# Kernel optimization log

Measured on AMD Instinct MI355X. Metric: run time of the kernel, lower is better.

The kernel has to match this reference:

```python
import jax, jax.numpy as jnp
import numpy as np

B, S = 256, 512          # batch, seqlen
M = 128                  # memory_size
DK = 128                 # memory_key_state_dim == q_embed_dim == final_fc_dim
DV = 256                 # memory_value_state_dim == qa_embed_dim
NQ = 10000               # n_question
FC = 128                 # final_fc_dim


def _kaiming(key, shape):
    fan_in = shape[-1]
    return jax.random.normal(key, shape, dtype=jnp.float32) * np.float32(np.sqrt(2.0 / fan_in))


def setup_inputs() -> dict:
    key = jax.random.key(0)
    ks = jax.random.split(key, 12)
    q_data = jax.random.randint(ks[0], (B, S), 0, NQ + 1)
    qa_data = jax.random.randint(ks[1], (B, S), 0, 2 * NQ + 1)
    # embedding tables (padding_idx=0 -> zero row)
    q_embed_table = _kaiming(ks[2], (NQ + 1, DK)).at[0].set(0.0)
    qa_embed_table = _kaiming(ks[3], (2 * NQ + 1, DV)).at[0].set(0.0)
    memory_key = _kaiming(ks[4], (M, DK))
    init_memory_value = _kaiming(ks[5], (M, DV))
    W_erase = _kaiming(ks[6], (DV, DV)); b_erase = jnp.zeros((DV,), jnp.float32)
    W_add = _kaiming(ks[7], (DV, DV)); b_add = jnp.zeros((DV,), jnp.float32)
    W_read = _kaiming(ks[8], (FC, DV + FC)); b_read = jnp.zeros((FC,), jnp.float32)
    W_pred = _kaiming(ks[9], (1, FC)); b_pred = jnp.zeros((1,), jnp.float32)
    return {
        "q_data": q_data, "qa_data": qa_data,
        "q_embed_table": q_embed_table, "qa_embed_table": qa_embed_table,
        "memory_key": memory_key, "init_memory_value": init_memory_value,
        "W_erase": W_erase, "b_erase": b_erase,
        "W_add": W_add, "b_add": b_add,
        "W_read": W_read, "b_read": b_read,
        "W_pred": W_pred, "b_pred": b_pred,
    }


def reference(q_data, qa_data, q_embed_table, qa_embed_table, memory_key,
              init_memory_value, W_erase, b_erase, W_add, b_add,
              W_read, b_read, W_pred, b_pred):
    batch = q_data.shape[0]
    qe = q_embed_table[q_data]      # [B,S,DK]
    qae = qa_embed_table[qa_data]   # [B,S,DV]

    def step(mem, inp):
        q_t, qa_t = inp  # [B,DK], [B,DV]
        # key addressing: tiny matmul + softmax
        w = jax.nn.softmax(q_t @ memory_key.T, axis=1)            # [B,M]
        # weighted read from value memory
        read = jnp.einsum('bm,bmd->bd', w, mem)                   # [B,DV]
        # gated erase/add write
        e = jax.nn.sigmoid(qa_t @ W_erase.T + b_erase)            # [B,DV]
        a = jnp.tanh(qa_t @ W_add.T + b_add)                      # [B,DV]
        mem = mem * (1.0 - w[:, :, None] * e[:, None, :]) + w[:, :, None] * a[:, None, :]
        return mem, read

    mem0 = jnp.broadcast_to(init_memory_value, (batch,) + init_memory_value.shape)
    _, reads = jax.lax.scan(step, mem0, (qe.transpose(1, 0, 2), qae.transpose(1, 0, 2)))
    reads = reads.transpose(1, 0, 2)                              # [B,S,DV]

    predict_input = jnp.concatenate([reads, qe], axis=-1)         # [B,S,DV+FC]
    h = jnp.tanh(predict_input @ W_read.T + b_read)               # [B,S,FC]
    logits = h @ W_pred.T + b_pred                                # [B,S,1]
    return logits[..., 0]
```

## Files before the change

kernel.cpp:

```cpp
#include <hip/hip_runtime.h>
#include <hip/hip_bf16.h>


#define BB    256
#define SS    512
#define MM    128
#define DKk   128
#define DVv   256

typedef float  f32x2  __attribute__((ext_vector_type(2)));
typedef float  f32x4  __attribute__((ext_vector_type(4)));
typedef short  bf16x8 __attribute__((ext_vector_type(8)));

static __device__ __forceinline__ unsigned short f2bf(float f) {
    unsigned u = __float_as_uint(f);
    unsigned r = (u + 0x7FFFu + ((u >> 16) & 1u)) >> 16;
    return (unsigned short)r;
}
static __device__ __forceinline__ float bf2f(unsigned short u) {
    return __uint_as_float(((unsigned)u) << 16);
}
static __device__ __forceinline__ float fast_tanh(float x) {
    float ex = __expf(2.f * x);
    return 1.f - 2.f / (ex + 1.f);
}
static __device__ __forceinline__ float fast_sigmoid(float x) {
    return 1.f / (1.f + __expf(-x));
}

__global__ __launch_bounds__(256) void kcvt(const float* __restrict__ qa_tab,
                                            const float* __restrict__ q_tab,
                                            const float* __restrict__ W_er,
                                            const float* __restrict__ W_ad,
                                            const float* __restrict__ W_rd,
                                            const float* __restrict__ mk,
                                            unsigned short* __restrict__ qa16,
                                            unsigned short* __restrict__ q16,
                                            unsigned short* __restrict__ wea16,
                                            unsigned short* __restrict__ wrd16,
                                            unsigned short* __restrict__ mk16,
                                            int n_qa, int n_q) {
    for (int i = blockIdx.x * 256 + threadIdx.x; i < n_qa; i += gridDim.x * 256)
        qa16[i] = f2bf(qa_tab[i]);
    for (int i = blockIdx.x * 256 + threadIdx.x; i < n_q; i += gridDim.x * 256)
        q16[i] = f2bf(q_tab[i]);
    for (int i = blockIdx.x * 256 + threadIdx.x; i < 65536; i += gridDim.x * 256) {
        wea16[i] = f2bf(W_er[i]);
        wea16[65536 + i] = f2bf(W_ad[i]);
    }
    for (int i = blockIdx.x * 256 + threadIdx.x; i < 49152; i += gridDim.x * 256)
        wrd16[i] = f2bf(W_rd[i]);
    for (int i = blockIdx.x * 256 + threadIdx.x; i < 16384; i += gridDim.x * 256)
        mk16[i] = f2bf(mk[i]);
}

__global__ __launch_bounds__(256) void k1_mfma(const int* __restrict__ q_data,
                                               const unsigned short* __restrict__ q16,
                                               const unsigned short* __restrict__ mk16,
                                               float* __restrict__ w_buf,
                                               int tcs, int tcm, int coff) {
    __shared__ __align__(16) unsigned short A_lds[128 * 64];
    __shared__ int qidx[128];
    int t = threadIdx.x;
    int row0 = blockIdx.x * 128;
    if (t < 128) {
        int rl = row0 + t;
        qidx[t] = q_data[(rl >> tcs) * SS + coff + (rl & tcm)];
    }
    int l = t & 63;
    int wid = t >> 6;
    f32x4 acc[2][8];
    #pragma unroll
    for (int i = 0; i < 2; ++i)
        #pragma unroll
        for (int j = 0; j < 8; ++j)
            acc[i][j] = (f32x4){0.f, 0.f, 0.f, 0.f};

    for (int ks = 0; ks < 128; ks += 64) {
        __syncthreads();
        #pragma unroll
        for (int p = 0; p < 4; ++p) {
            int U = p * 256 + t;
            int r = U >> 3, kb = U & 7;
            int kb_log = kb ^ (r & 7);
            int4 v = *reinterpret_cast<const int4*>(q16 + (size_t)qidx[r] * DKk + ks + kb_log * 8);
            *reinterpret_cast<int4*>(&A_lds[U * 8]) = v;
        }
        __syncthreads();
        #pragma unroll
        for (int ksub = 0; ksub < 2; ++ksub) {
            bf16x8 af[2];
            #pragma unroll
            for (int mi = 0; mi < 2; ++mi) {
                int r = wid * 32 + mi * 16 + (l & 15);
                int kb_log = ksub * 4 + (l >> 4);
                int pu = r * 8 + (kb_log ^ (r & 7));
                af[mi] = *reinterpret_cast<const bf16x8*>(&A_lds[pu * 8]);
            }
            #pragma unroll
            for (int nj = 0; nj < 8; ++nj) {
                int col = nj * 16 + (l & 15);
                bf16x8 bf = *reinterpret_cast<const bf16x8*>(
                    mk16 + (size_t)col * DKk + ks + ksub * 32 + (l >> 4) * 8);
                #pragma unroll
                for (int mi = 0; mi < 2; ++mi)
                    acc[mi][nj] = __builtin_amdgcn_mfma_f32_16x16x32_bf16(af[mi], bf, acc[mi][nj], 0, 0, 0);
            }
        }
    }
    #pragma unroll
    for (int mi = 0; mi < 2; ++mi) {
        #pragma unroll
        for (int reg = 0; reg < 4; ++reg) {
            float mx = acc[mi][0][reg];
            #pragma unroll
            for (int nj = 1; nj < 8; ++nj) mx = fmaxf(mx, acc[mi][nj][reg]);
            #pragma unroll
            for (int off = 1; off < 16; off <<= 1) mx = fmaxf(mx, __shfl_xor(mx, off, 64));
            float p[8], s = 0.f;
            #pragma unroll
            for (int nj = 0; nj < 8; ++nj) { p[nj] = __expf(acc[mi][nj][reg] - mx); s += p[nj]; }
            #pragma unroll
            for (int off = 1; off < 16; off <<= 1) s += __shfl_xor(s, off, 64);
            float inv = 1.f / s;
            int row = row0 + wid * 32 + mi * 16 + (l >> 4) * 4 + reg;
            #pragma unroll
            for (int nj = 0; nj < 8; ++nj)
                w_buf[(size_t)row * MM + nj * 16 + (l & 15)] = p[nj] * inv;
        }
    }
}

__global__ __launch_bounds__(256) void k2_ea_mfma(const int* __restrict__ qa_data,
                                                  const unsigned short* __restrict__ qa16,
                                                  const unsigned short* __restrict__ wea16,
                                                  const float* __restrict__ b_er,
                                                  const float* __restrict__ b_ad,
                                                  unsigned short* __restrict__ ea16,
                                                  int tcs, int tcm, int coff) {
    __shared__ __align__(16) unsigned short A_lds[128 * 64];
    __shared__ int qidx[128];
    int t = threadIdx.x;
    int rb = blockIdx.x >> 2, cb = blockIdx.x & 3;
    int row0 = rb * 128;
    if (t < 128) {
        int rl = row0 + t;
        qidx[t] = qa_data[(rl >> tcs) * SS + coff + (rl & tcm)];
    }
    int l = t & 63;
    int wid = t >> 6, wr = wid >> 1, wc = wid & 1;
    f32x4 acc[4][4];
    #pragma unroll
    for (int i = 0; i < 4; ++i)
        #pragma unroll
        for (int j = 0; j < 4; ++j)
            acc[i][j] = (f32x4){0.f, 0.f, 0.f, 0.f};

    for (int ks = 0; ks < 256; ks += 64) {
        __syncthreads();
        #pragma unroll
        for (int p = 0; p < 4; ++p) {
            int U = p * 256 + t;
            int r = U >> 3, kb = U & 7;
            int kb_log = kb ^ (r & 7);
            int4 v = *reinterpret_cast<const int4*>(qa16 + (size_t)qidx[r] * 256 + ks + kb_log * 8);
            *reinterpret_cast<int4*>(&A_lds[U * 8]) = v;
        }
        __syncthreads();
        #pragma unroll
        for (int ksub = 0; ksub < 2; ++ksub) {
            bf16x8 af[4];
            #pragma unroll
            for (int mi = 0; mi < 4; ++mi) {
                int r = wr * 64 + mi * 16 + (l & 15);
                int kb_log = ksub * 4 + (l >> 4);
                int pu = r * 8 + (kb_log ^ (r & 7));
                af[mi] = *reinterpret_cast<const bf16x8*>(&A_lds[pu * 8]);
            }
            #pragma unroll
            for (int nj = 0; nj < 4; ++nj) {
                int col = cb * 128 + wc * 64 + nj * 16 + (l & 15);
                bf16x8 bf = *reinterpret_cast<const bf16x8*>(
                    wea16 + (size_t)col * 256 + ks + ksub * 32 + (l >> 4) * 8);
                #pragma unroll
                for (int mi = 0; mi < 4; ++mi)
                    acc[mi][nj] = __builtin_amdgcn_mfma_f32_16x16x32_bf16(af[mi], bf, acc[mi][nj], 0, 0, 0);
            }
        }
    }
    #pragma unroll
    for (int nj = 0; nj < 4; ++nj) {
        int col = cb * 128 + wc * 64 + nj * 16 + (l & 15);
        bool is_e = (cb < 2);
        float bias = is_e ? b_er[col] : b_ad[col - 256];
        #pragma unroll
        for (int mi = 0; mi < 4; ++mi) {
            #pragma unroll
            for (int reg = 0; reg < 4; ++reg) {
                int rl = row0 + wr * 64 + mi * 16 + (l >> 4) * 4 + reg;
                float x = acc[mi][nj][reg] + bias;
                float y = is_e ? fast_sigmoid(x) : fast_tanh(x);
                ea16[(size_t)rl * 512 + col] = f2bf(y);
            }
        }
    }
}

__global__ __launch_bounds__(1024, 8) void k3_seq(const float* __restrict__ w_buf,
                                                  const unsigned short* __restrict__ ea16,
                                                  const float* __restrict__ init_mem,
                                                  float* __restrict__ state,
                                                  unsigned short* __restrict__ reads16,
                                                  int TC, int first, int last) {
    __shared__ float rdlds[8][8][128];
    int b    = blockIdx.x >> 1;
    int half = blockIdx.x & 1;
    int tid = threadIdx.x;
    int wv = tid >> 6, lane = tid & 63;
    int mq = wv >> 1;
    int dh = wv & 1;
    int dl = dh * 64 + lane;
    int d  = half * 128 + dl;
    int m0 = mq * 16;
    f32x2 mem[8];
    if (first) {
        #pragma unroll
        for (int i = 0; i < 8; ++i) {
            mem[i].x = init_mem[(size_t)(m0 + 2 * i) * DVv + d];
            mem[i].y = init_mem[(size_t)(m0 + 2 * i + 1) * DVv + d];
        }
    } else {
        #pragma unroll
        for (int i = 0; i < 8; ++i)
            mem[i] = *reinterpret_cast<const f32x2*>(&state[((size_t)b * DVv + d) * MM + m0 + 2 * i]);
    }
    size_t rb = (size_t)b * TC;
    unsigned wrow = (unsigned)__builtin_amdgcn_readfirstlane((int)((unsigned)rb * MM + m0));
    const f32x2* wbase2 = reinterpret_cast<const f32x2*>(w_buf + wrow);
    int tcl = TC - 1;

    f32x2 wA[8], wB[8];
    #pragma unroll
    for (int j = 0; j < 8; ++j) wA[j] = wbase2[j];
    #pragma unroll
    for (int j = 0; j < 8; ++j) wB[j] = wbase2[64 + j];

    for (int t0 = 0; t0 < TC; t0 += 8) {
        float e8[8], a8[8];
        #pragma unroll
        for (int g = 0; g < 8; ++g) {
            const unsigned short* ep = ea16 + (rb + t0 + g) * 512;
            e8[g] = bf2f(ep[d]);
            a8[g] = bf2f(ep[256 + d]);
        }
        #define K3_STEP(G, WCUR)                                                              \
        {                                                                                     \
            f32x2 rd; rd.x = 0.f; rd.y = 0.f;                                                 \
            f32x2 ne2; ne2.x = -e8[G]; ne2.y = -e8[G];                                        \
            f32x2 a2;  a2.x = a8[G];  a2.y = a8[G];                                           \
            _Pragma("unroll")                                                                 \
            for (int i = 0; i < 8; ++i) {                                                     \
                f32x2 tt;                                                                     \
                asm("v_pk_fma_f32 %0, %1, %2, %0" : "+v"(rd)     : "s"(WCUR[i]), "v"(mem[i]));\
                asm("v_pk_fma_f32 %0, %1, %2, %3" : "=v"(tt)     : "v"(ne2), "v"(mem[i]), "v"(a2)); \
                asm("v_pk_fma_f32 %0, %1, %2, %0" : "+v"(mem[i]) : "s"(WCUR[i]), "v"(tt));    \
            }                                                                                 \
            rdlds[G][mq][dl] = rd.x + rd.y;                                                   \
            int tp = t0 + G + 2; tp = (tp < tcl) ? tp : tcl;                                  \
            _Pragma("unroll")                                                                 \
            for (int j = 0; j < 8; ++j) WCUR[j] = wbase2[tp * 64 + j];                        \
        }
        K3_STEP(0, wA) K3_STEP(1, wB) K3_STEP(2, wA) K3_STEP(3, wB)
        K3_STEP(4, wA) K3_STEP(5, wB) K3_STEP(6, wA) K3_STEP(7, wB)
        #undef K3_STEP
        __syncthreads();
        {
            int g = tid >> 7, dd = tid & 127;
            float s = rdlds[g][0][dd] + rdlds[g][1][dd] + rdlds[g][2][dd] + rdlds[g][3][dd]
                    + rdlds[g][4][dd] + rdlds[g][5][dd] + rdlds[g][6][dd] + rdlds[g][7][dd];
            reads16[(rb + t0 + g) * DVv + half * 128 + dd] = f2bf(s);
        }
        __syncthreads();
    }
    if (!last) {
        #pragma unroll
        for (int i = 0; i < 8; ++i)
            *reinterpret_cast<f32x2*>(&state[((size_t)b * DVv + d) * MM + m0 + 2 * i]) = mem[i];
    }
}

__global__ __launch_bounds__(256) void k4_mfma(const int* __restrict__ q_data,
                                               const unsigned short* __restrict__ q16,
                                               const unsigned short* __restrict__ reads16,
                                               const unsigned short* __restrict__ wrd16,
                                               const float* __restrict__ b_rd,
                                               const float* __restrict__ W_pr,
                                               const float* __restrict__ b_pr,
                                               float* __restrict__ out,
                                               int tcs, int tcm, int coff) {
    __shared__ __align__(16) unsigned short A_lds[128 * 64];
    __shared__ int qidx[128];
    __shared__ float plds[2][128];
    int t = threadIdx.x;
    int row0 = blockIdx.x * 128;
    if (t < 128) {
        int rl = row0 + t;
        qidx[t] = q_data[(rl >> tcs) * SS + coff + (rl & tcm)];
    }
    int l = t & 63;
    int wid = t >> 6, wr = wid >> 1, wc = wid & 1;
    f32x4 acc[4][4];
    #pragma unroll
    for (int i = 0; i < 4; ++i)
        #pragma unroll
        for (int j = 0; j < 4; ++j)
            acc[i][j] = (f32x4){0.f, 0.f, 0.f, 0.f};

    for (int ks = 0; ks < 384; ks += 64) {
        __syncthreads();
        #pragma unroll
        for (int p = 0; p < 4; ++p) {
            int U = p * 256 + t;
            int r = U >> 3, kb = U & 7;
            int kb_log = kb ^ (r & 7);
            int kg = ks + kb_log * 8;
            const unsigned short* src = (kg < 256)
                ? (reads16 + (size_t)(row0 + r) * DVv + kg)
                : (q16 + (size_t)qidx[r] * DKk + (kg - 256));
            int4 v = *reinterpret_cast<const int4*>(src);
            *reinterpret_cast<int4*>(&A_lds[U * 8]) = v;
        }
        __syncthreads();
        #pragma unroll
        for (int ksub = 0; ksub < 2; ++ksub) {
            bf16x8 af[4];
            #pragma unroll
            for (int mi = 0; mi < 4; ++mi) {
                int r = wr * 64 + mi * 16 + (l & 15);
                int kb_log = ksub * 4 + (l >> 4);
                int pu = r * 8 + (kb_log ^ (r & 7));
                af[mi] = *reinterpret_cast<const bf16x8*>(&A_lds[pu * 8]);
            }
            #pragma unroll
            for (int nj = 0; nj < 4; ++nj) {
                int col = wc * 64 + nj * 16 + (l & 15);
                bf16x8 bf = *reinterpret_cast<const bf16x8*>(
                    wrd16 + (size_t)col * 384 + ks + ksub * 32 + (l >> 4) * 8);
                #pragma unroll
                for (int mi = 0; mi < 4; ++mi)
                    acc[mi][nj] = __builtin_amdgcn_mfma_f32_16x16x32_bf16(af[mi], bf, acc[mi][nj], 0, 0, 0);
            }
        }
    }
    float part[16];
    #pragma unroll
    for (int k = 0; k < 16; ++k) part[k] = 0.f;
    #pragma unroll
    for (int nj = 0; nj < 4; ++nj) {
        int col = wc * 64 + nj * 16 + (l & 15);
        float bias = b_rd[col];
        float wpr = W_pr[col];
        #pragma unroll
        for (int mi = 0; mi < 4; ++mi) {
            #pragma unroll
            for (int reg = 0; reg < 4; ++reg) {
                float h = fast_tanh(acc[mi][nj][reg] + bias);
                part[mi * 4 + reg] = fmaf(h, wpr, part[mi * 4 + reg]);
            }
        }
    }
    #pragma unroll
    for (int k = 0; k < 16; ++k) {
        #pragma unroll
        for (int off = 1; off < 16; off <<= 1)
            part[k] += __shfl_xor(part[k], off, 64);
    }
    if ((l & 15) == 0) {
        #pragma unroll
        for (int mi = 0; mi < 4; ++mi)
            #pragma unroll
            for (int reg = 0; reg < 4; ++reg) {
                int row = wr * 64 + mi * 16 + (l >> 4) * 4 + reg;
                plds[wc][row] = part[mi * 4 + reg];
            }
    }
    __syncthreads();
    if (t < 128) {
        float s = plds[0][t] + plds[1][t] + b_pr[0];
        int rl = row0 + t;
        out[(rl >> tcs) * SS + coff + (rl & tcm)] = s;
    }
}

extern "C" void kernel_launch(void* const* d_in, const int* in_sizes, int n_in,
                              void* d_out, int out_size, void* d_ws, size_t ws_size,
                              hipStream_t stream) {
    const int*   q_data   = (const int*)d_in[0];
    const int*   qa_data  = (const int*)d_in[1];
    const float* q_tab    = (const float*)d_in[2];
    const float* qa_tab   = (const float*)d_in[3];
    const float* mk       = (const float*)d_in[4];
    const float* init_mem = (const float*)d_in[5];
    const float* W_er     = (const float*)d_in[6];
    const float* b_er     = (const float*)d_in[7];
    const float* W_ad     = (const float*)d_in[8];
    const float* b_ad     = (const float*)d_in[9];
    const float* W_rd     = (const float*)d_in[10];
    const float* b_rd     = (const float*)d_in[11];
    const float* W_pr     = (const float*)d_in[12];
    const float* b_pr     = (const float*)d_in[13];
    float* out = (float*)d_out;

    const size_t state_f = (size_t)BB * MM * DVv;
    const size_t qa16_n  = (size_t)in_sizes[3];
    const size_t q16_n   = (size_t)in_sizes[2];
    const size_t wea16_n = 131072;
    const size_t wrd16_n = 49152;
    const size_t mk16_n  = 16384;
    const size_t bf16_f  = (qa16_n + q16_n + wea16_n + wrd16_n + mk16_n) / 2 + 32;

    size_t avail_f = ws_size / 4;
    int TC = 8;
    {
        const int cand[] = {256, 128, 64, 32, 16, 8};
        for (int i = 0; i < 6; ++i) {
            size_t need = state_f + bf16_f + (size_t)BB * cand[i] * (MM + 256 + 128);
            if (need <= avail_f) { TC = cand[i]; break; }
        }
    }
    int NC = SS / TC;
    int tcs = __builtin_ctz(TC);
    int tcm = TC - 1;

    float* ws      = (float*)d_ws;
    float* state   = ws;
    float* w_buf   = state + state_f;
    unsigned short* ea16    = (unsigned short*)(w_buf + (size_t)BB * TC * MM);
    unsigned short* reads16 = ea16 + (size_t)BB * TC * 512;
    unsigned short* qa16  = reads16 + (size_t)BB * TC * DVv;
    unsigned short* q16   = qa16 + qa16_n;
    unsigned short* wea16 = q16 + q16_n;
    unsigned short* wrd16 = wea16 + wea16_n;
    unsigned short* mk16  = wrd16 + wrd16_n;

    kcvt<<<1024, 256, 0, stream>>>(qa_tab, q_tab, W_er, W_ad, W_rd, mk,
                                   qa16, q16, wea16, wrd16, mk16,
                                   (int)qa16_n, (int)q16_n);
    for (int c = 0; c < NC; ++c) {
        int coff = c * TC;
        int rows = BB * TC;
        k2_ea_mfma<<<(rows / 128) * 4, 256, 0, stream>>>(qa_data, qa16, wea16, b_er, b_ad,
                                                         ea16, tcs, tcm, coff);
        k1_mfma<<<rows / 128, 256, 0, stream>>>(q_data, q16, mk16, w_buf, tcs, tcm, coff);
        k3_seq<<<2 * BB, 1024, 0, stream>>>(w_buf, ea16, init_mem, state, reads16,
                                            TC, c == 0, c == NC - 1);
        k4_mfma<<<rows / 128, 256, 0, stream>>>(q_data, q16, reads16, wrd16, b_rd, W_pr, b_pr,
                                                out, tcs, tcm, coff);
    }
}
```

Measured before the change: 595.0 us.

## Reduce k3 read partials with wave shuffles instead of LDS and block barriers

Restructures the sequential memory-update kernel from 1024-thread blocks (two per batch row) to 256-thread blocks (eight per batch row). The lane layout changes so that all eight m-slices of a d column sit in one wave. Per-step read partial sums are now combined with xor shuffles inside the wave, which removes the LDS buffer and both __syncthreads per 8-step group. The cost is that attention weights become per-lane vector loads (VGPR operands) instead of uniform scalar loads, so register and memory traffic for w rises.

Measured after the change: 913.9 us. 53.6% more time.

```diff
diff --git a/kernel.cpp b/kernel.cpp
--- a/kernel.cpp
+++ b/kernel.cpp
@@ -206,21 +206,19 @@
     }
 }
 
-__global__ __launch_bounds__(1024, 8) void k3_seq(const float* __restrict__ w_buf,
-                                                  const unsigned short* __restrict__ ea16,
-                                                  const float* __restrict__ init_mem,
-                                                  float* __restrict__ state,
-                                                  unsigned short* __restrict__ reads16,
-                                                  int TC, int first, int last) {
-    __shared__ float rdlds[8][8][128];
-    int b    = blockIdx.x >> 1;
-    int half = blockIdx.x & 1;
+__global__ __launch_bounds__(256, 6) void k3_seq(const float* __restrict__ w_buf,
+                                                 const unsigned short* __restrict__ ea16,
+                                                 const float* __restrict__ init_mem,
+                                                 float* __restrict__ state,
+                                                 unsigned short* __restrict__ reads16,
+                                                 int TC, int first, int last) {
     int tid = threadIdx.x;
     int wv = tid >> 6, lane = tid & 63;
-    int mq = wv >> 1;
-    int dh = wv & 1;
-    int dl = dh * 64 + lane;
-    int d  = half * 128 + dl;
+    int b    = blockIdx.x >> 3;
+    int dblk = blockIdx.x & 7;
+    int mq   = lane >> 3;
+    int dsub = lane & 7;
+    int d  = dblk * 32 + wv * 8 + dsub;
     int m0 = mq * 16;
     f32x2 mem[8];
     if (first) {
@@ -235,15 +233,19 @@
             mem[i] = *reinterpret_cast<const f32x2*>(&state[((size_t)b * DVv + d) * MM + m0 + 2 * i]);
     }
     size_t rb = (size_t)b * TC;
-    unsigned wrow = (unsigned)__builtin_amdgcn_readfirstlane((int)((unsigned)rb * MM + m0));
-    const f32x2* wbase2 = reinterpret_cast<const f32x2*>(w_buf + wrow);
     int tcl = TC - 1;
 
     f32x2 wA[8], wB[8];
-    #pragma unroll
-    for (int j = 0; j < 8; ++j) wA[j] = wbase2[j];
-    #pragma unroll
-    for (int j = 0; j < 8; ++j) wB[j] = wbase2[64 + j];
+    #define WLOAD(WARR, T)                                                                  \
+    {                                                                                       \
+        const float* wsrc = w_buf + (rb + (size_t)(T)) * MM + m0;                           \
+        *reinterpret_cast<f32x4*>(&WARR[0]) = *reinterpret_cast<const f32x4*>(wsrc);        \
+        *reinterpret_cast<f32x4*>(&WARR[2]) = *reinterpret_cast<const f32x4*>(wsrc + 4);    \
+        *reinterpret_cast<f32x4*>(&WARR[4]) = *reinterpret_cast<const f32x4*>(wsrc + 8);    \
+        *reinterpret_cast<f32x4*>(&WARR[6]) = *reinterpret_cast<const f32x4*>(wsrc + 12);   \
+    }
+    WLOAD(wA, 0)
+    WLOAD(wB, 1)
 
     for (int t0 = 0; t0 < TC; t0 += 8) {
         float e8[8], a8[8];
@@ -253,6 +255,7 @@
             e8[g] = bf2f(ep[d]);
             a8[g] = bf2f(ep[256 + d]);
         }
+        float rds[8];
         #define K3_STEP(G, WCUR)                                                              \
         {                                                                                     \
             f32x2 rd; rd.x = 0.f; rd.y = 0.f;                                                 \
@@ -261,27 +264,32 @@
             _Pragma("unroll")                                                                 \
             for (int i = 0; i < 8; ++i) {                                                     \
                 f32x2 tt;                                                                     \
-                asm("v_pk_fma_f32 %0, %1, %2, %0" : "+v"(rd)     : "s"(WCUR[i]), "v"(mem[i]));\
+                asm("v_pk_fma_f32 %0, %1, %2, %0" : "+v"(rd)     : "v"(WCUR[i]), "v"(mem[i]));\
                 asm("v_pk_fma_f32 %0, %1, %2, %3" : "=v"(tt)     : "v"(ne2), "v"(mem[i]), "v"(a2)); \
-                asm("v_pk_fma_f32 %0, %1, %2, %0" : "+v"(mem[i]) : "s"(WCUR[i]), "v"(tt));    \
+                asm("v_pk_fma_f32 %0, %1, %2, %0" : "+v"(mem[i]) : "v"(WCUR[i]), "v"(tt));    \
             }                                                                                 \
-            rdlds[G][mq][dl] = rd.x + rd.y;                                                   \
+            rds[G] = rd.x + rd.y;                                                             \
             int tp = t0 + G + 2; tp = (tp < tcl) ? tp : tcl;                                  \
-            _Pragma("unroll")                                                                 \
-            for (int j = 0; j < 8; ++j) WCUR[j] = wbase2[tp * 64 + j];                        \
+            WLOAD(WCUR, tp)                                                                   \
         }
         K3_STEP(0, wA) K3_STEP(1, wB) K3_STEP(2, wA) K3_STEP(3, wB)
         K3_STEP(4, wA) K3_STEP(5, wB) K3_STEP(6, wA) K3_STEP(7, wB)
         #undef K3_STEP
-        __syncthreads();
-        {
-            int g = tid >> 7, dd = tid & 127;
-            float s = rdlds[g][0][dd] + rdlds[g][1][dd] + rdlds[g][2][dd] + rdlds[g][3][dd]
-                    + rdlds[g][4][dd] + rdlds[g][5][dd] + rdlds[g][6][dd] + rdlds[g][7][dd];
-            reads16[(rb + t0 + g) * DVv + half * 128 + dd] = f2bf(s);
-        }
-        __syncthreads();
-    }
+        #pragma unroll
+        for (int g = 0; g < 8; ++g) {
+            float v = rds[g];
+            v += __shfl_xor(v, 8, 64);
+            v += __shfl_xor(v, 16, 64);
+            v += __shfl_xor(v, 32, 64);
+            rds[g] = v;
+        }
+        if (mq == 0) {
+            #pragma unroll
+            for (int g = 0; g < 8; ++g)
+                reads16[(rb + t0 + g) * DVv + d] = f2bf(rds[g]);
+        }
+    }
+    #undef WLOAD
     if (!last) {
         #pragma unroll
         for (int i = 0; i < 8; ++i)
@@ -452,8 +460,8 @@
         k2_ea_mfma<<<(rows / 128) * 4, 256, 0, stream>>>(qa_data, qa16, wea16, b_er, b_ad,
                                                          ea16, tcs, tcm, coff);
         k1_mfma<<<rows / 128, 256, 0, stream>>>(q_data, q16, mk16, w_buf, tcs, tcm, coff);
-        k3_seq<<<2 * BB, 1024, 0, stream>>>(w_buf, ea16, init_mem, state, reads16,
-                                            TC, c == 0, c == NC - 1);
+        k3_seq<<<8 * BB, 256, 0, stream>>>(w_buf, ea16, init_mem, state, reads16,
+                                           TC, c == 0, c == NC - 1);
         k4_mfma<<<rows / 128, 256, 0, stream>>>(q_data, q16, reads16, wrd16, b_rd, W_pr, b_pr,
                                                 out, tcs, tcm, coff);
     }
```

## Interleave erase/add in one dword and split sequential kernel into quarter-D blocks

Applied to the files above, without the earlier changes.

The erase/add producer now writes negated erase and add values interleaved per column. The sequential memory kernel can then fetch both with a single 32-bit load and feed them to a packed FMA through op_sel, which removes the separate broadcasts. The sequential kernel moves from 512 blocks of 1024 threads to 1024 blocks of 512 threads, each block covering 64 value dims. The attention-weight prefetch depth goes from 2 to 4 steps to hide load latency. The risks are the inline-asm op_sel encoding and the extra registers held by the deeper prefetch buffers.

Result: faster. 542.8 us (-8.8%).

```diff
diff --git a/kernel.cpp b/kernel.cpp
--- a/kernel.cpp
+++ b/kernel.cpp
@@ -16,9 +16,6 @@
     unsigned u = __float_as_uint(f);
     unsigned r = (u + 0x7FFFu + ((u >> 16) & 1u)) >> 16;
     return (unsigned short)r;
-}
-static __device__ __forceinline__ float bf2f(unsigned short u) {
-    return __uint_as_float(((unsigned)u) << 16);
 }
 static __device__ __forceinline__ float fast_tanh(float x) {
     float ex = __expf(2.f * x);
@@ -199,28 +196,26 @@
             for (int reg = 0; reg < 4; ++reg) {
                 int rl = row0 + wr * 64 + mi * 16 + (l >> 4) * 4 + reg;
                 float x = acc[mi][nj][reg] + bias;
-                float y = is_e ? fast_sigmoid(x) : fast_tanh(x);
-                ea16[(size_t)rl * 512 + col] = f2bf(y);
-            }
-        }
-    }
-}
-
-__global__ __launch_bounds__(1024, 8) void k3_seq(const float* __restrict__ w_buf,
-                                                  const unsigned short* __restrict__ ea16,
-                                                  const float* __restrict__ init_mem,
-                                                  float* __restrict__ state,
-                                                  unsigned short* __restrict__ reads16,
-                                                  int TC, int first, int last) {
-    __shared__ float rdlds[8][8][128];
-    int b    = blockIdx.x >> 1;
-    int half = blockIdx.x & 1;
+                float y = is_e ? -fast_sigmoid(x) : fast_tanh(x);
+                int idx = is_e ? (2 * col) : (2 * (col - 256) + 1);
+                ea16[(size_t)rl * 512 + idx] = f2bf(y);
+            }
+        }
+    }
+}
+
+__global__ __launch_bounds__(512, 8) void k3_seq(const float* __restrict__ w_buf,
+                                                 const unsigned short* __restrict__ ea16,
+                                                 const float* __restrict__ init_mem,
+                                                 float* __restrict__ state,
+                                                 unsigned short* __restrict__ reads16,
+                                                 int TC, int first, int last) {
+    __shared__ float rdlds[8][8][64];
     int tid = threadIdx.x;
-    int wv = tid >> 6, lane = tid & 63;
-    int mq = wv >> 1;
-    int dh = wv & 1;
-    int dl = dh * 64 + lane;
-    int d  = half * 128 + dl;
+    int mq = tid >> 6, lane = tid & 63;
+    int b  = blockIdx.x >> 2;
+    int dq = blockIdx.x & 3;
+    int d  = dq * 64 + lane;
     int m0 = mq * 16;
     f32x2 mem[8];
     if (first) {
@@ -235,53 +230,55 @@
             mem[i] = *reinterpret_cast<const f32x2*>(&state[((size_t)b * DVv + d) * MM + m0 + 2 * i]);
     }
     size_t rb = (size_t)b * TC;
-    unsigned wrow = (unsigned)__builtin_amdgcn_readfirstlane((int)((unsigned)rb * MM + m0));
+    const unsigned* ea32 = reinterpret_cast<const unsigned*>(ea16);
+    unsigned wrow = (unsigned)__builtin_amdgcn_readfirstlane((int)((unsigned)(rb * MM) + m0));
     const f32x2* wbase2 = reinterpret_cast<const f32x2*>(w_buf + wrow);
     int tcl = TC - 1;
 
-    f32x2 wA[8], wB[8];
-    #pragma unroll
-    for (int j = 0; j < 8; ++j) wA[j] = wbase2[j];
-    #pragma unroll
-    for (int j = 0; j < 8; ++j) wB[j] = wbase2[64 + j];
+    f32x2 wA[8], wB[8], wC[8], wD[8];
+    #define WLOAD(W, T)                                                             \
+    {                                                                               \
+        _Pragma("unroll")                                                           \
+        for (int j = 0; j < 8; ++j) W[j] = wbase2[(size_t)(T) * 64 + j];            \
+    }
+    WLOAD(wA, 0) WLOAD(wB, 1) WLOAD(wC, 2) WLOAD(wD, 3)
 
     for (int t0 = 0; t0 < TC; t0 += 8) {
-        float e8[8], a8[8];
-        #pragma unroll
-        for (int g = 0; g < 8; ++g) {
-            const unsigned short* ep = ea16 + (rb + t0 + g) * 512;
-            e8[g] = bf2f(ep[d]);
-            a8[g] = bf2f(ep[256 + d]);
-        }
+        unsigned u8[8];
+        #pragma unroll
+        for (int g = 0; g < 8; ++g)
+            u8[g] = ea32[(rb + t0 + g) * 256 + d];
         #define K3_STEP(G, WCUR)                                                              \
         {                                                                                     \
+            f32x2 EA;                                                                         \
+            EA.x = __uint_as_float(u8[G] << 16);                                      \
+            EA.y = __uint_as_float(u8[G] & 0xffff0000u);                              \
             f32x2 rd; rd.x = 0.f; rd.y = 0.f;                                                 \
-            f32x2 ne2; ne2.x = -e8[G]; ne2.y = -e8[G];                                        \
-            f32x2 a2;  a2.x = a8[G];  a2.y = a8[G];                                           \
             _Pragma("unroll")                                                                 \
             for (int i = 0; i < 8; ++i) {                                                     \
                 f32x2 tt;                                                                     \
-                asm("v_pk_fma_f32 %0, %1, %2, %0" : "+v"(rd)     : "s"(WCUR[i]), "v"(mem[i]));\
-                asm("v_pk_fma_f32 %0, %1, %2, %3" : "=v"(tt)     : "v"(ne2), "v"(mem[i]), "v"(a2)); \
+                asm("v_pk_fma_f32 %0, %1, %2, %0" : "+v"(rd) : "s"(WCUR[i]), "v"(mem[i]));    \
+                asm("v_pk_fma_f32 %0, %1, %2, %1 op_sel:[0,0,1] op_sel_hi:[0,1,1]"            \
+                    : "=v"(tt) : "v"(EA), "v"(mem[i]));                                       \
                 asm("v_pk_fma_f32 %0, %1, %2, %0" : "+v"(mem[i]) : "s"(WCUR[i]), "v"(tt));    \
             }                                                                                 \
-            rdlds[G][mq][dl] = rd.x + rd.y;                                                   \
-            int tp = t0 + G + 2; tp = (tp < tcl) ? tp : tcl;                                  \
-            _Pragma("unroll")                                                                 \
-            for (int j = 0; j < 8; ++j) WCUR[j] = wbase2[tp * 64 + j];                        \
-        }
-        K3_STEP(0, wA) K3_STEP(1, wB) K3_STEP(2, wA) K3_STEP(3, wB)
-        K3_STEP(4, wA) K3_STEP(5, wB) K3_STEP(6, wA) K3_STEP(7, wB)
+            rdlds[G][mq][lane] = rd.x + rd.y;                                                 \
+            int tp = t0 + G + 4; tp = (tp < tcl) ? tp : tcl;                                  \
+            WLOAD(WCUR, tp)                                                                   \
+        }
+        K3_STEP(0, wA) K3_STEP(1, wB) K3_STEP(2, wC) K3_STEP(3, wD)
+        K3_STEP(4, wA) K3_STEP(5, wB) K3_STEP(6, wC) K3_STEP(7, wD)
         #undef K3_STEP
         __syncthreads();
         {
-            int g = tid >> 7, dd = tid & 127;
-            float s = rdlds[g][0][dd] + rdlds[g][1][dd] + rdlds[g][2][dd] + rdlds[g][3][dd]
-                    + rdlds[g][4][dd] + rdlds[g][5][dd] + rdlds[g][6][dd] + rdlds[g][7][dd];
-            reads16[(rb + t0 + g) * DVv + half * 128 + dd] = f2bf(s);
-        }
-        __syncthreads();
-    }
+            int g = tid >> 6, dl = tid & 63;
+            float s = rdlds[g][0][dl] + rdlds[g][1][dl] + rdlds[g][2][dl] + rdlds[g][3][dl]
+                    + rdlds[g][4][dl] + rdlds[g][5][dl] + rdlds[g][6][dl] + rdlds[g][7][dl];
+            reads16[(rb + t0 + g) * DVv + dq * 64 + dl] = f2bf(s);
+        }
+        __syncthreads();
+    }
+    #undef WLOAD
     if (!last) {
         #pragma unroll
         for (int i = 0; i < 8; ++i)
@@ -452,8 +449,8 @@
         k2_ea_mfma<<<(rows / 128) * 4, 256, 0, stream>>>(qa_data, qa16, wea16, b_er, b_ad,
                                                          ea16, tcs, tcm, coff);
         k1_mfma<<<rows / 128, 256, 0, stream>>>(q_data, q16, mk16, w_buf, tcs, tcm, coff);
-        k3_seq<<<2 * BB, 1024, 0, stream>>>(w_buf, ea16, init_mem, state, reads16,
-                                            TC, c == 0, c == NC - 1);
+        k3_seq<<<4 * BB, 512, 0, stream>>>(w_buf, ea16, init_mem, state, reads16,
+                                           TC, c == 0, c == NC - 1);
         k4_mfma<<<rows / 128, 256, 0, stream>>>(q_data, q16, reads16, wrd16, b_rd, W_pr, b_pr,
                                                 out, tcs, tcm, coff);
     }
```
